# Kernel tuning notes

Hardware: AMD Instinct MI355X
Metric: run time of the kernel (lower is better)

The kernel has to match this reference:

```python
import jax, jax.numpy as jnp
import numpy as np

T, I, O = 10000, 2048, 512
DT = 0.001
PSP_DECAY = float(np.exp(-DT / 0.02))
OUT_DECAY = float(np.exp(-DT / 0.01))
STDP_C = 1.0
STDP_MU = 0.1
SPIKE_PROB = 0.05


def setup_inputs() -> dict:
    key = jax.random.key(0)
    k1, k2, k3 = jax.random.split(key, 3)
    # Poisson-encoded binary spike trains (as produced by SpikePopulationGroupBatchToTimeEncoder)
    input_spikes = (jax.random.uniform(k1, (T, I)) < SPIKE_PROB).astype(jnp.float32)
    u_rand = jax.random.uniform(k2, (T,), dtype=jnp.float32)  # per-step WTA sampling uniforms
    W = 0.1 * jax.random.normal(k3, (O, I), dtype=jnp.float32)
    b = jnp.zeros((O,), jnp.float32)
    return {"input_spikes": input_spikes, "u_rand": u_rand, "W": W, "b": b}


def _input_psp(spikes):
    # exponential PSP filter along time: psp[t] = decay*psp[t-1] + spikes[t]
    def step(c, s):
        c = PSP_DECAY * c + s
        return c, c
    _, psps = jax.lax.scan(step, jnp.zeros(spikes.shape[1], spikes.dtype), spikes)
    return psps  # [T, I]


def reference(input_spikes, u_rand, W, b):
    psps = _input_psp(input_spikes)
    n_out = W.shape[0]

    def step(carry, inp):
        W, b, trace = carry
        psp, u = inp
        z_in = W @ psp + b                              # linear, [O]
        p = jax.nn.softmax(z_in)                        # stochastic WTA cell
        idx = jnp.minimum(jnp.sum(jnp.cumsum(p) < u), n_out - 1)
        z_out = jax.nn.one_hot(idx, n_out, dtype=psp.dtype)
        trace = OUT_DECAY * trace + z_out               # neuron cell state
        # Bayesian STDP (sequential, depends on previous step's weights)
        dW = z_out[:, None] * (STDP_C * jnp.exp(-W) * psp[None, :] - 1.0)
        db = z_out * (STDP_C * jnp.exp(-b) - 1.0)
        return (W + STDP_MU * dW, b + STDP_MU * db, trace), z_out

    (Wf, bf, trace), z_outs = jax.lax.scan(
        step, (W, b, jnp.zeros_like(b)), (psps, u_rand))
    # matches torch forward's (stacked z_out, final z_state)
    return z_outs, trace
```

## Files before the change

### kernel.cpp

```cpp
#include <hip/hip_runtime.h>
#include <math.h>

static constexpr int T_STEPS = 10000;
static constexpr int I_DIM = 2048;
static constexpr int O_DIM = 512;
static constexpr int NWG = 4;
static constexpr int STRIPE = 128;
static constexpr int WGS = 512;
static constexpr int KPAD = 192;
static constexpr int GN = 16;
static constexpr float PSPD = 0.9512294245007140091f;
static constexpr float OUTD = 0.9048374180359595732f;
static constexpr float MU = 0.1f;

typedef float __attribute__((ext_vector_type(4))) f32x4;
typedef float __attribute__((ext_vector_type(2))) f32x2;

static constexpr size_t WT_BLK = (size_t)(I_DIM + 1) * STRIPE;

__global__ void build_idx_kernel(const float* __restrict__ spikes,
                                 unsigned short* __restrict__ idxl,
                                 int* __restrict__ cnts) {
    int t = blockIdx.x;
    int tid = threadIdx.x;
    if (t >= T_STEPS) {
        for (int p = tid; p < KPAD; p += 256) idxl[(size_t)t * KPAD + p] = (unsigned short)I_DIM;
        if (tid == 0) cnts[t] = 0;
        return;
    }
    const float4* row = reinterpret_cast<const float4*>(spikes + (size_t)t * I_DIM);
    float4 a = row[tid * 2];
    float4 b = row[tid * 2 + 1];
    float v[8] = {a.x, a.y, a.z, a.w, b.x, b.y, b.z, b.w};
    unsigned short tmp[8];
    int c = 0;
#pragma unroll
    for (int j = 0; j < 8; ++j)
        if (v[j] != 0.0f) tmp[c++] = (unsigned short)(tid * 8 + j);

    int lane = tid & 63, wid = tid >> 6;
    int x = c;
    for (int d = 1; d < 64; d <<= 1) {
        int y = __shfl_up(x, d);
        if (lane >= d) x += y;
    }
    __shared__ int wtot[4];
    if (lane == 63) wtot[wid] = x;
    __syncthreads();
    int off = x - c;
    for (int w = 0; w < wid; ++w) off += wtot[w];
    int tot = wtot[0] + wtot[1] + wtot[2] + wtot[3];
    if (tot > KPAD) tot = KPAD;
    for (int j = 0; j < c; ++j) {
        int p = off + j;
        if (p < KPAD) idxl[(size_t)t * KPAD + p] = tmp[j];
    }
    for (int p = tid; p < KPAD; p += 256)
        if (p >= tot) idxl[(size_t)t * KPAD + p] = (unsigned short)I_DIM;
    if (tid == 0) cnts[t] = tot;
}

__global__ void copy_w_kernel(const float* __restrict__ W, float* __restrict__ Wrow) {
    int i = blockIdx.x * blockDim.x + threadIdx.x;
    reinterpret_cast<float4*>(Wrow)[i] = reinterpret_cast<const float4*>(W)[i];
}

__global__ void transpose_kernel(const float* __restrict__ W, float* __restrict__ Wt) {
    __shared__ float tile[32][33];
    int i0 = blockIdx.x * 32;
    int o0 = blockIdx.y * 32;
    int x = threadIdx.x;
    for (int y = threadIdx.y; y < 32; y += 8)
        tile[y][x] = W[(size_t)(o0 + y) * I_DIM + i0 + x];
    __syncthreads();
    for (int y = threadIdx.y; y < 32; y += 8) {
        int o = o0 + x, i = i0 + y;
        Wt[(size_t)(o >> 7) * WT_BLK + (size_t)i * STRIPE + (o & 127)] = tile[x][y];
    }
}

__global__ void zero_pad_row_kernel(float* __restrict__ Wt) {
    int w = threadIdx.x >> 7, c = threadIdx.x & 127;
    Wt[(size_t)w * WT_BLK + (size_t)I_DIM * STRIPE + c] = 0.0f;
}

__device__ __forceinline__ void bar() {
    asm volatile("s_waitcnt lgkmcnt(0)" ::: "memory");
    __builtin_amdgcn_sched_barrier(0);
    __builtin_amdgcn_s_barrier();
    __builtin_amdgcn_sched_barrier(0);
}

__device__ __forceinline__ float wave_max_dpp(float x) {
    int xb = __float_as_int(x);
#define DPPSTEPM(ctrl, rm)                                                          \
    {                                                                               \
        int tt = __builtin_amdgcn_update_dpp(0xff800000, xb, ctrl, rm, 0xf, false); \
        xb = __float_as_int(fmaxf(__int_as_float(xb), __int_as_float(tt)));         \
    }
    DPPSTEPM(0x111, 0xf)
    DPPSTEPM(0x112, 0xf)
    DPPSTEPM(0x114, 0xf)
    DPPSTEPM(0x118, 0xf)
    DPPSTEPM(0x142, 0xa)
    DPPSTEPM(0x143, 0xc)
#undef DPPSTEPM
    return __int_as_float(__builtin_amdgcn_readlane(xb, 63));
}

__device__ __forceinline__ float dpp_scan_add(float x) {
#define DPPSTEPA(ctrl, rm)                                                          \
    {                                                                               \
        float tt = __int_as_float(                                                  \
            __builtin_amdgcn_update_dpp(0, __float_as_int(x), ctrl, rm, 0xf, false)); \
        x += tt;                                                                    \
    }
    DPPSTEPA(0x111, 0xf)
    DPPSTEPA(0x112, 0xf)
    DPPSTEPA(0x114, 0xf)
    DPPSTEPA(0x118, 0xf)
    DPPSTEPA(0x142, 0xa)
    DPPSTEPA(0x143, 0xc)
#undef DPPSTEPA
    return x;
}

__launch_bounds__(WGS, 1)
__global__ void seq_kernel(const unsigned short* __restrict__ idxl,
                           const int* __restrict__ cnts,
                           const float* __restrict__ u_rand,
                           const float* __restrict__ b_in,
                           float* __restrict__ Wrow,
                           float* __restrict__ Wt,
                           unsigned long long* __restrict__ slots,
                           float* __restrict__ out) {
    __shared__ __align__(16) float psp[I_DIM + 4];
    __shared__ __align__(16) float mk0[I_DIM + 4];
    __shared__ __align__(16) float mk1[I_DIM + 4];
    __shared__ f32x2 sg[8][64];
    __shared__ float redE[8], redF[8], redG[2][8];
    __shared__ unsigned short sidx[3][KPAD];
    __shared__ int s_rr, s_own;

    const int w = blockIdx.x;
    const int tid = threadIdx.x;
    const int lane = tid & 63;
    const int jw = tid >> 6;
    const int i4 = tid * 4;
    const int o0 = w * STRIPE;
    float* __restrict__ WtS = Wt + (size_t)w * WT_BLK;
    const unsigned long long wt_base = (unsigned long long)WtS;

    for (int p = tid; p < I_DIM + 4; p += WGS) { psp[p] = 0.0f; mk0[p] = 0.0f; mk1[p] = 0.0f; }
    for (int p = tid; p < 3 * KPAD; p += WGS) ((unsigned short*)sidx)[p] = idxl[p];
    if (tid == 0) { s_rr = 0; s_own = 0; }
    __syncthreads();
    const int cnt0 = cnts[0];
    if (tid < KPAD) {
        psp[sidx[0][tid]] = 1.0f;
        mk1[sidx[1][tid]] = 1.0f;
    }
    __syncthreads();
    {
        float a0 = 0.0f, a1 = 0.0f;
        for (int k = jw; k < cnt0; k += 8) {
            int col = sidx[0][k];
            f32x2 v = *(const f32x2*)(WtS + (size_t)col * STRIPE + lane * 2);
            a0 += v.x; a1 += v.y;
        }
        sg[jw][lane] = (f32x2){a0, a1};
    }
    float aA0 = 0.0f, aA1 = 0.0f, b0 = 0.0f, b1 = 0.0f, tr0 = 0.0f, tr1 = 0.0f;
    if (jw == 0) { b0 = b_in[o0 + 2 * lane]; b1 = b_in[o0 + 2 * lane + 1]; }
    int own1 = 0, own2 = 0, col1 = 0, col2 = 0;
    float nw0 = 0.0f, nw1 = 0.0f, nw2 = 0.0f, nw3 = 0.0f;
    int cnt_use = cnts[1];
    float u_cur = u_rand[0];
    __syncthreads();

    for (int t = 0; t < T_STEPS; ++t) {
        const int par = t & 1;
        float* mcur = par ? mk1 : mk0;
        float* mnxt = par ? mk0 : mk1;

        float u_nxt; int cnt_fut;
        {
            const float* up = u_rand + (t + 1 < T_STEPS ? t + 1 : T_STEPS - 1);
            asm volatile("global_load_dword %0, %1, off" : "=&v"(u_nxt) : "v"(up) : "memory");
            const int* cp = cnts + (t + 2);
            asm volatile("global_load_dword %0, %1, off" : "=&v"(cnt_fut) : "v"(cp) : "memory");
        }
        unsigned int pfw = 0;
        if (tid >= 256 && tid < 256 + KPAD / 2) {
            const unsigned int* pp = reinterpret_cast<const unsigned int*>(idxl) +
                                     (size_t)(t + 3) * (KPAD / 2) + (tid - 256);
            asm volatile("global_load_dword %0, %1, off" : "=&v"(pfw) : "v"(pp) : "memory");
        }
        f32x2 vals[GN];
        {
            const unsigned short* lst = sidx[(t + 1) % 3];
#pragma unroll
            for (int j = 0; j < GN; ++j) {
                int col = lst[jw + 8 * j];
                unsigned int voff = ((unsigned)col << 9) | ((unsigned)lane << 3);
                asm volatile("global_load_dwordx2 %0, %1, %2"
                             : "=&v"(vals[j]) : "v"(voff), "s"(wt_base) : "memory");
            }
        }
        f32x4 mreg = *(const f32x4*)(mnxt + i4);
        if (own1) {
            float gp2 = nw0 * mreg.x + nw1 * mreg.y + nw2 * mreg.z + nw3 * mreg.w;
            float gs = dpp_scan_add(gp2);
            if (lane == 63) redG[par][jw] = gs;
        }
        *(f32x4*)(mcur + i4) = (f32x4){0.0f, 0.0f, 0.0f, 0.0f};

        float e0 = 0.0f, e1 = 0.0f, pin = 0.0f, pex = 0.0f, m_w = 0.0f, S_w = 0.0f;
        if (jw == 0) {
            tr0 *= OUTD; tr1 *= OUTD;
            float v0 = 0.0f, v1 = 0.0f;
#pragma unroll
            for (int j = 0; j < 8; ++j) { f32x2 s = sg[j][lane]; v0 += s.x; v1 += s.y; }
            if (own1) {
                float es = 0.0f, fs = 0.0f;
#pragma unroll
                for (int j = 0; j < 8; ++j) { es += redE[j]; fs += redF[j]; }
                if (lane == (col1 >> 1)) {
                    if (col1 & 1) { aA1 += es; v1 = fs; } else { aA0 += es; v0 = fs; }
                }
            }
            if (own2 && !(own1 && col2 == col1)) {
                float gs = 0.0f;
#pragma unroll
                for (int j = 0; j < 8; ++j) gs += redG[par ^ 1][j];
                if (lane == (col2 >> 1)) { if (col2 & 1) v1 = gs; else v0 = gs; }
            }
            aA0 = PSPD * aA0 + v0; aA1 = PSPD * aA1 + v1;
            float z0 = aA0 + b0, z1 = aA1 + b1;
            m_w = wave_max_dpp(fmaxf(z0, z1));
            e0 = expf(z0 - m_w); e1 = expf(z1 - m_w);
            pin = dpp_scan_add(e0 + e1);
            pex = __int_as_float(
                __builtin_amdgcn_update_dpp(0, __float_as_int(pin), 0x111, 0xf, 0xf, false));
            float p15 = __int_as_float(__builtin_amdgcn_readlane(__float_as_int(pin), 15));
            float p31 = __int_as_float(__builtin_amdgcn_readlane(__float_as_int(pin), 31));
            float p47 = __int_as_float(__builtin_amdgcn_readlane(__float_as_int(pin), 47));
            if (lane == 16) pex = p15;
            if (lane == 32) pex = p31;
            if (lane == 48) pex = p47;
            S_w = __int_as_float(__builtin_amdgcn_readlane(__float_as_int(pin), 63));
            unsigned long long tag = ((unsigned long long)(unsigned)(t + 1)) << 32;
            if (lane == 0) {
                unsigned long long* my = slots + (((size_t)par * NWG + w) * 2);
                __hip_atomic_store(my + 0, tag | (unsigned)__float_as_int(m_w),
                                   __ATOMIC_RELAXED, __HIP_MEMORY_SCOPE_AGENT);
                __hip_atomic_store(my + 1, tag | (unsigned)__float_as_int(S_w),
                                   __ATOMIC_RELAXED, __HIP_MEMORY_SCOPE_AGENT);
            }
            int oi = lane >> 1; oi += (oi >= w) ? 1 : 0; oi &= 3;
            unsigned long long* sp = slots + (((size_t)par * NWG + oi) * 2 + (lane & 1));
            bool need = (lane < 6);
            unsigned long long want = (unsigned long long)(unsigned)(t + 1);
            unsigned long long got = 0;
            bool ok = !need;
            int it = 0;
            while (!__all(ok)) {
                if (!ok) {
                    got = __hip_atomic_load(sp, __ATOMIC_RELAXED, __HIP_MEMORY_SCOPE_AGENT);
                    ok = ((got >> 32) == want);
                }
                if (++it > (1 << 21)) break;
            }
            float pay = __int_as_float((int)(unsigned)got);
            float mj[4], sj[4];
#pragma unroll
            for (int j = 0; j < 4; ++j) {
                if (j == w) { mj[j] = m_w; sj[j] = S_w; }
                else {
                    int pos = j - (j > w ? 1 : 0);
                    mj[j] = __shfl(pay, 2 * pos);
                    sj[j] = __shfl(pay, 2 * pos + 1);
                }
            }
            float M = fmaxf(fmaxf(mj[0], mj[1]), fmaxf(mj[2], mj[3]));
            float o_run = 0.0f, offw = 0.0f, offn = 0.0f, sc_w = 0.0f;
#pragma unroll
            for (int j = 0; j < 4; ++j) {
                float sc = expf(mj[j] - M);
                if (j == w) { offw = o_run; sc_w = sc; }
                o_run = fmaf(sj[j], sc, o_run);
                if (j == w) offn = o_run;
            }
            float uQ = u_cur * o_run;
            int owner = (((offw < uQ) || w == 0) && ((uQ <= offn) || w == NWG - 1)) ? 1 : 0;
            if (lane == 0) { s_own = owner; s_rr = STRIPE - 1; }
            if (owner) {
                float cqp0 = fmaf(pex, sc_w, offw);
                float cq0  = fmaf(pex + e0, sc_w, offw);
                float cq1  = fmaf(pin, sc_w, offw);
                bool firstG = (w == 0 && lane == 0);
                bool lastG  = (w == NWG - 1 && lane == 63);
                bool w0c = (cqp0 < uQ || firstG) && (uQ <= cq0);
                bool w1c = (cq0 < uQ) && (uQ <= cq1 || lastG);
                if (w0c) s_rr = 2 * lane;
                if (w1c) s_rr = 2 * lane + 1;
            }
        }
        bar();

        const int rr = s_rr;
        const int own = s_own;
        const int rrglob = o0 + rr;
        f32x4 w2 = (f32x4){0.0f, 0.0f, 0.0f, 0.0f};
        if (own) {
            const float* rp = Wrow + (size_t)rrglob * I_DIM + i4;
            asm volatile("global_load_dwordx4 %0, %1, off" : "=&v"(w2) : "v"(rp) : "memory");
        }
        asm volatile("s_waitcnt vmcnt(0)" ::: "memory");
        __builtin_amdgcn_sched_barrier(0);
        asm volatile("" : "+v"(cnt_fut), "+v"(u_nxt));
        {
            float a0 = vals[0].x, a1 = vals[0].y;
#pragma unroll
            for (int j = 1; j < GN; ++j) { a0 += vals[j].x; a1 += vals[j].y; }
            if (cnt_use > 8 * GN) {
                const unsigned short* lst = sidx[(t + 1) % 3];
                for (int k = 8 * GN + jw; k < cnt_use; k += 8) {
                    int col = lst[k];
                    f32x2 v = *(const f32x2*)(WtS + (size_t)col * STRIPE + lane * 2);
                    a0 += v.x; a1 += v.y;
                }
            }
            sg[jw][lane] = (f32x2){a0, a1};
        }
        if (tid >= 256 && tid < 256 + KPAD / 2)
            ((unsigned int*)sidx[(t + 3) % 3])[tid - 256] = pfw;
        if (tid < KPAD) mcur[sidx[(t + 2) % 3][tid]] = 1.0f;
        f32x4 pr = *(const f32x4*)(psp + i4);
        if (own) {
            nw0 = w2.x + MU * (expf(-w2.x) * pr.x - 1.0f);
            nw1 = w2.y + MU * (expf(-w2.y) * pr.y - 1.0f);
            nw2 = w2.z + MU * (expf(-w2.z) * pr.z - 1.0f);
            nw3 = w2.w + MU * (expf(-w2.w) * pr.w - 1.0f);
            *(f32x4*)(Wrow + (size_t)rrglob * I_DIM + i4) = (f32x4){nw0, nw1, nw2, nw3};
            WtS[(size_t)(i4 + 0) * STRIPE + rr] = nw0;
            WtS[(size_t)(i4 + 1) * STRIPE + rr] = nw1;
            WtS[(size_t)(i4 + 2) * STRIPE + rr] = nw2;
            WtS[(size_t)(i4 + 3) * STRIPE + rr] = nw3;
            float dp = (nw0 - w2.x) * pr.x + (nw1 - w2.y) * pr.y +
                       (nw2 - w2.z) * pr.z + (nw3 - w2.w) * pr.w;
            float gp = nw0 * mreg.x + nw1 * mreg.y + nw2 * mreg.z + nw3 * mreg.w;
            float ds = dpp_scan_add(dp);
            float gs = dpp_scan_add(gp);
            if (lane == 63) { redE[jw] = ds; redF[jw] = gs; }
            if (jw == 0 && lane == (rr >> 1)) {
                if (rr & 1) { tr1 += 1.0f; b1 = b1 + MU * (expf(-b1) - 1.0f); }
                else        { tr0 += 1.0f; b0 = b0 + MU * (expf(-b0) - 1.0f); }
                out[(size_t)t * O_DIM + rrglob] = 1.0f;
            }
        }
        {
#pragma clang fp contract(off)
            float q0 = pr.x * PSPD; q0 += mreg.x;
            float q1 = pr.y * PSPD; q1 += mreg.y;
            float q2 = pr.z * PSPD; q2 += mreg.z;
            float q3 = pr.w * PSPD; q3 += mreg.w;
            *(f32x4*)(psp + i4) = (f32x4){q0, q1, q2, q3};
        }
        own2 = own1; col2 = col1;
        own1 = own;  col1 = rr;
        cnt_use = cnt_fut;
        u_cur = u_nxt;
        bar();
    }

    if (jw == 0) {
        out[(size_t)T_STEPS * O_DIM + o0 + 2 * lane] = tr0;
        out[(size_t)T_STEPS * O_DIM + o0 + 2 * lane + 1] = tr1;
    }
}

extern "C" void kernel_launch(void* const* d_in, const int* in_sizes, int n_in,
                              void* d_out, int out_size, void* d_ws, size_t ws_size,
                              hipStream_t stream) {
    const float* spikes = (const float*)d_in[0];
    const float* u_rand = (const float*)d_in[1];
    const float* W      = (const float*)d_in[2];
    const float* b      = (const float*)d_in[3];
    float* out = (float*)d_out;

    float* Wrow = (float*)d_ws;
    float* Wt   = Wrow + (size_t)O_DIM * I_DIM;
    unsigned short* idxl = (unsigned short*)(Wt + (size_t)NWG * WT_BLK);
    int* cnts = (int*)(idxl + (size_t)(T_STEPS + 4) * KPAD);
    unsigned long long* slots = (unsigned long long*)(cnts + (T_STEPS + 4));

    hipMemsetAsync(d_out, 0, (size_t)out_size * sizeof(float), stream);
    hipMemsetAsync(slots, 0, 2 * NWG * 2 * sizeof(unsigned long long), stream);

    hipLaunchKernelGGL(build_idx_kernel, dim3(T_STEPS + 4), dim3(256), 0, stream,
                       spikes, idxl, cnts);
    hipLaunchKernelGGL(copy_w_kernel, dim3((O_DIM * I_DIM / 4) / 256), dim3(256), 0, stream,
                       W, Wrow);
    hipLaunchKernelGGL(transpose_kernel, dim3(I_DIM / 32, O_DIM / 32), dim3(32, 8), 0, stream,
                       W, Wt);
    hipLaunchKernelGGL(zero_pad_row_kernel, dim3(1), dim3(NWG * STRIPE), 0, stream, Wt);
    hipLaunchKernelGGL(seq_kernel, dim3(NWG), dim3(WGS), 0, stream,
                       idxl, cnts, u_rand, b, Wrow, Wt, slots, out);
}
```

Baseline: 34.54 ms.

## Dedicate wave 0 to softmax/WTA while seven waves gather next-step partial sums

The per-step work is split by wave. Wave 0 only does the softmax, the cross-workgroup exchange and the WTA sampling. The other seven waves gather the next step's sparse weight-column sums into a double-buffered shared array, and they also do the PSP and mask updates before the barrier. This moves the gather and the PSP update off the critical path after the barrier, so they overlap with wave 0's serial reduction and spin-wait. In exchange, the gather is spread over fewer waves, each doing more loads per step (GN raised to 19), and the spin-wait iteration limit is doubled.

```diff
diff --git a/kernel.cpp b/kernel.cpp
--- a/kernel.cpp
+++ b/kernel.cpp
@@ -8,7 +8,8 @@
 static constexpr int STRIPE = 128;
 static constexpr int WGS = 512;
 static constexpr int KPAD = 192;
-static constexpr int GN = 16;
+static constexpr int NSPL = 7;
+static constexpr int GN = 19;
 static constexpr float PSPD = 0.9512294245007140091f;
 static constexpr float OUTD = 0.9048374180359595732f;
 static constexpr float MU = 0.1f;
@@ -137,7 +138,7 @@
     __shared__ __align__(16) float psp[I_DIM + 4];
     __shared__ __align__(16) float mk0[I_DIM + 4];
     __shared__ __align__(16) float mk1[I_DIM + 4];
-    __shared__ f32x2 sg[8][64];
+    __shared__ f32x2 sg[2][NSPL][64];
     __shared__ float redE[8], redF[8], redG[2][8];
     __shared__ unsigned short sidx[3][KPAD];
     __shared__ int s_rr, s_own;
@@ -161,14 +162,14 @@
         mk1[sidx[1][tid]] = 1.0f;
     }
     __syncthreads();
-    {
+    if (jw > 0) {
         float a0 = 0.0f, a1 = 0.0f;
-        for (int k = jw; k < cnt0; k += 8) {
+        for (int k = jw - 1; k < cnt0; k += NSPL) {
             int col = sidx[0][k];
             f32x2 v = *(const f32x2*)(WtS + (size_t)col * STRIPE + lane * 2);
             a0 += v.x; a1 += v.y;
         }
-        sg[jw][lane] = (f32x2){a0, a1};
+        sg[0][jw - 1][lane] = (f32x2){a0, a1};
     }
     float aA0 = 0.0f, aA1 = 0.0f, b0 = 0.0f, b1 = 0.0f, tr0 = 0.0f, tr1 = 0.0f;
     if (jw == 0) { b0 = b_in[o0 + 2 * lane]; b1 = b_in[o0 + 2 * lane + 1]; }
@@ -180,6 +181,8 @@
 
     for (int t = 0; t < T_STEPS; ++t) {
         const int par = t & 1;
+        const int cb = par;
+        const int nb = par ^ 1;
         float* mcur = par ? mk1 : mk0;
         float* mnxt = par ? mk0 : mk1;
 
@@ -196,31 +199,62 @@
                                      (size_t)(t + 3) * (KPAD / 2) + (tid - 256);
             asm volatile("global_load_dword %0, %1, off" : "=&v"(pfw) : "v"(pp) : "memory");
         }
-        f32x2 vals[GN];
-        {
-            const unsigned short* lst = sidx[(t + 1) % 3];
-#pragma unroll
-            for (int j = 0; j < GN; ++j) {
-                int col = lst[jw + 8 * j];
-                unsigned int voff = ((unsigned)col << 9) | ((unsigned)lane << 3);
-                asm volatile("global_load_dwordx2 %0, %1, %2"
-                             : "=&v"(vals[j]) : "v"(voff), "s"(wt_base) : "memory");
-            }
-        }
-        f32x4 mreg = *(const f32x4*)(mnxt + i4);
-        if (own1) {
-            float gp2 = nw0 * mreg.x + nw1 * mreg.y + nw2 * mreg.z + nw3 * mreg.w;
-            float gs = dpp_scan_add(gp2);
-            if (lane == 63) redG[par][jw] = gs;
-        }
-        *(f32x4*)(mcur + i4) = (f32x4){0.0f, 0.0f, 0.0f, 0.0f};
-
-        float e0 = 0.0f, e1 = 0.0f, pin = 0.0f, pex = 0.0f, m_w = 0.0f, S_w = 0.0f;
-        if (jw == 0) {
+        f32x4 mreg = (f32x4){0.0f, 0.0f, 0.0f, 0.0f};
+        f32x4 pr = (f32x4){0.0f, 0.0f, 0.0f, 0.0f};
+
+        if (jw > 0) {
+            f32x2 vals[GN];
+            {
+                const unsigned short* lst = sidx[(t + 1) % 3];
+                const int kw = jw - 1;
+#pragma unroll
+                for (int j = 0; j < GN; ++j) {
+                    int col = lst[kw + NSPL * j];
+                    unsigned int voff = ((unsigned)col << 9) | ((unsigned)lane << 3);
+                    asm volatile("global_load_dwordx2 %0, %1, %2"
+                                 : "=&v"(vals[j]) : "v"(voff), "s"(wt_base) : "memory");
+                }
+            }
+            mreg = *(const f32x4*)(mnxt + i4);
+            if (own1) {
+                float gp2 = nw0 * mreg.x + nw1 * mreg.y + nw2 * mreg.z + nw3 * mreg.w;
+                float gs = dpp_scan_add(gp2);
+                if (lane == 63) redG[par][jw] = gs;
+            }
+            *(f32x4*)(mcur + i4) = (f32x4){0.0f, 0.0f, 0.0f, 0.0f};
+            pr = *(const f32x4*)(psp + i4);
+            {
+#pragma clang fp contract(off)
+                float q0 = pr.x * PSPD; q0 += mreg.x;
+                float q1 = pr.y * PSPD; q1 += mreg.y;
+                float q2 = pr.z * PSPD; q2 += mreg.z;
+                float q3 = pr.w * PSPD; q3 += mreg.w;
+                *(f32x4*)(psp + i4) = (f32x4){q0, q1, q2, q3};
+            }
+            asm volatile("s_waitcnt vmcnt(0)" ::: "memory");
+            __builtin_amdgcn_sched_barrier(0);
+            asm volatile("" : "+v"(cnt_fut), "+v"(u_nxt));
+            {
+                float a0 = vals[0].x, a1 = vals[0].y;
+#pragma unroll
+                for (int j = 1; j < GN; ++j) { a0 += vals[j].x; a1 += vals[j].y; }
+                if (cnt_use > NSPL * GN) {
+                    const unsigned short* lst = sidx[(t + 1) % 3];
+                    for (int k = NSPL * GN + (jw - 1); k < cnt_use; k += NSPL) {
+                        int col = lst[k];
+                        f32x2 v = *(const f32x2*)(WtS + (size_t)col * STRIPE + lane * 2);
+                        a0 += v.x; a1 += v.y;
+                    }
+                }
+                sg[nb][jw - 1][lane] = (f32x2){a0, a1};
+            }
+            if (tid >= 256 && tid < 256 + KPAD / 2)
+                ((unsigned int*)sidx[(t + 3) % 3])[tid - 256] = pfw;
+        } else {
             tr0 *= OUTD; tr1 *= OUTD;
             float v0 = 0.0f, v1 = 0.0f;
 #pragma unroll
-            for (int j = 0; j < 8; ++j) { f32x2 s = sg[j][lane]; v0 += s.x; v1 += s.y; }
+            for (int j = 0; j < NSPL; ++j) { f32x2 s = sg[cb][j][lane]; v0 += s.x; v1 += s.y; }
             if (own1) {
                 float es = 0.0f, fs = 0.0f;
 #pragma unroll
@@ -237,10 +271,10 @@
             }
             aA0 = PSPD * aA0 + v0; aA1 = PSPD * aA1 + v1;
             float z0 = aA0 + b0, z1 = aA1 + b1;
-            m_w = wave_max_dpp(fmaxf(z0, z1));
-            e0 = expf(z0 - m_w); e1 = expf(z1 - m_w);
-            pin = dpp_scan_add(e0 + e1);
-            pex = __int_as_float(
+            float m_w = wave_max_dpp(fmaxf(z0, z1));
+            float e0 = expf(z0 - m_w), e1 = expf(z1 - m_w);
+            float pin = dpp_scan_add(e0 + e1);
+            float pex = __int_as_float(
                 __builtin_amdgcn_update_dpp(0, __float_as_int(pin), 0x111, 0xf, 0xf, false));
             float p15 = __int_as_float(__builtin_amdgcn_readlane(__float_as_int(pin), 15));
             float p31 = __int_as_float(__builtin_amdgcn_readlane(__float_as_int(pin), 31));
@@ -248,7 +282,7 @@
             if (lane == 16) pex = p15;
             if (lane == 32) pex = p31;
             if (lane == 48) pex = p47;
-            S_w = __int_as_float(__builtin_amdgcn_readlane(__float_as_int(pin), 63));
+            float S_w = __int_as_float(__builtin_amdgcn_readlane(__float_as_int(pin), 63));
             unsigned long long tag = ((unsigned long long)(unsigned)(t + 1)) << 32;
             if (lane == 0) {
                 unsigned long long* my = slots + (((size_t)par * NWG + w) * 2);
@@ -269,7 +303,7 @@
                     got = __hip_atomic_load(sp, __ATOMIC_RELAXED, __HIP_MEMORY_SCOPE_AGENT);
                     ok = ((got >> 32) == want);
                 }
-                if (++it > (1 << 21)) break;
+                if (++it > (1 << 22)) break;
             }
             float pay = __int_as_float((int)(unsigned)got);
             float mj[4], sj[4];
@@ -305,6 +339,25 @@
                 if (w0c) s_rr = 2 * lane;
                 if (w1c) s_rr = 2 * lane + 1;
             }
+            asm volatile("s_waitcnt vmcnt(0)" ::: "memory");
+            __builtin_amdgcn_sched_barrier(0);
+            asm volatile("" : "+v"(cnt_fut), "+v"(u_nxt));
+            mreg = *(const f32x4*)(mnxt + i4);
+            if (own1) {
+                float gp2 = nw0 * mreg.x + nw1 * mreg.y + nw2 * mreg.z + nw3 * mreg.w;
+                float gs = dpp_scan_add(gp2);
+                if (lane == 63) redG[par][0] = gs;
+            }
+            *(f32x4*)(mcur + i4) = (f32x4){0.0f, 0.0f, 0.0f, 0.0f};
+            pr = *(const f32x4*)(psp + i4);
+            {
+#pragma clang fp contract(off)
+                float q0 = pr.x * PSPD; q0 += mreg.x;
+                float q1 = pr.y * PSPD; q1 += mreg.y;
+                float q2 = pr.z * PSPD; q2 += mreg.z;
+                float q3 = pr.w * PSPD; q3 += mreg.w;
+                *(f32x4*)(psp + i4) = (f32x4){q0, q1, q2, q3};
+            }
         }
         bar();
 
@@ -316,28 +369,10 @@
             const float* rp = Wrow + (size_t)rrglob * I_DIM + i4;
             asm volatile("global_load_dwordx4 %0, %1, off" : "=&v"(w2) : "v"(rp) : "memory");
         }
-        asm volatile("s_waitcnt vmcnt(0)" ::: "memory");
-        __builtin_amdgcn_sched_barrier(0);
-        asm volatile("" : "+v"(cnt_fut), "+v"(u_nxt));
-        {
-            float a0 = vals[0].x, a1 = vals[0].y;
-#pragma unroll
-            for (int j = 1; j < GN; ++j) { a0 += vals[j].x; a1 += vals[j].y; }
-            if (cnt_use > 8 * GN) {
-                const unsigned short* lst = sidx[(t + 1) % 3];
-                for (int k = 8 * GN + jw; k < cnt_use; k += 8) {
-                    int col = lst[k];
-                    f32x2 v = *(const f32x2*)(WtS + (size_t)col * STRIPE + lane * 2);
-                    a0 += v.x; a1 += v.y;
-                }
-            }
-            sg[jw][lane] = (f32x2){a0, a1};
-        }
-        if (tid >= 256 && tid < 256 + KPAD / 2)
-            ((unsigned int*)sidx[(t + 3) % 3])[tid - 256] = pfw;
         if (tid < KPAD) mcur[sidx[(t + 2) % 3][tid]] = 1.0f;
-        f32x4 pr = *(const f32x4*)(psp + i4);
         if (own) {
+            asm volatile("s_waitcnt vmcnt(0)" ::: "memory");
+            __builtin_amdgcn_sched_barrier(0);
             nw0 = w2.x + MU * (expf(-w2.x) * pr.x - 1.0f);
             nw1 = w2.y + MU * (expf(-w2.y) * pr.y - 1.0f);
             nw2 = w2.z + MU * (expf(-w2.z) * pr.z - 1.0f);
@@ -359,14 +394,6 @@
                 out[(size_t)t * O_DIM + rrglob] = 1.0f;
             }
         }
-        {
-#pragma clang fp contract(off)
-            float q0 = pr.x * PSPD; q0 += mreg.x;
-            float q1 = pr.y * PSPD; q1 += mreg.y;
-            float q2 = pr.z * PSPD; q2 += mreg.z;
-            float q3 = pr.w * PSPD; q3 += mreg.w;
-            *(f32x4*)(psp + i4) = (f32x4){q0, q1, q2, q3};
-        }
         own2 = own1; col2 = col1;
         own1 = own;  col1 = rr;
         cnt_use = cnt_fut;
```

Result: faster. 27.75 ms (-19.6%).

## Collapse four-workgroup split into single 1024-thread workgroup, dropping global-memory handshakes

Applied to the files above, without the earlier changes.

Replaces the four cooperating workgroups, which exchanged per-step softmax max/sum through global atomic slots with spin-waits, with one 1024-thread workgroup that does the whole output dimension and reduces through shared memory and barriers. Work inside the block is specialised: 12 waves gather transposed weight rows with dwordx4 loads over six splits, and 4 waves do softmax and sampling, with winner selection via shared atomicMin. This removes cross-CU polling latency on every sequential step. In exchange, one CU now carries all gather bandwidth and weight-update work, so per-step compute and memory issue are less parallel.

```diff
diff --git a/kernel.cpp b/kernel.cpp
--- a/kernel.cpp
+++ b/kernel.cpp
@@ -4,19 +4,16 @@
 static constexpr int T_STEPS = 10000;
 static constexpr int I_DIM = 2048;
 static constexpr int O_DIM = 512;
-static constexpr int NWG = 4;
-static constexpr int STRIPE = 128;
-static constexpr int WGS = 512;
+static constexpr int WGS = 1024;
 static constexpr int KPAD = 192;
-static constexpr int GN = 16;
+static constexpr int NSPL = 6;
+static constexpr int GN = 19;
 static constexpr float PSPD = 0.9512294245007140091f;
 static constexpr float OUTD = 0.9048374180359595732f;
 static constexpr float MU = 0.1f;
 
 typedef float __attribute__((ext_vector_type(4))) f32x4;
 typedef float __attribute__((ext_vector_type(2))) f32x2;
-
-static constexpr size_t WT_BLK = (size_t)(I_DIM + 1) * STRIPE;
 
 __global__ void build_idx_kernel(const float* __restrict__ spikes,
                                  unsigned short* __restrict__ idxl,
@@ -73,15 +70,12 @@
     for (int y = threadIdx.y; y < 32; y += 8)
         tile[y][x] = W[(size_t)(o0 + y) * I_DIM + i0 + x];
     __syncthreads();
-    for (int y = threadIdx.y; y < 32; y += 8) {
-        int o = o0 + x, i = i0 + y;
-        Wt[(size_t)(o >> 7) * WT_BLK + (size_t)i * STRIPE + (o & 127)] = tile[x][y];
-    }
+    for (int y = threadIdx.y; y < 32; y += 8)
+        Wt[(size_t)(i0 + y) * O_DIM + o0 + x] = tile[x][y];
 }
 
 __global__ void zero_pad_row_kernel(float* __restrict__ Wt) {
-    int w = threadIdx.x >> 7, c = threadIdx.x & 127;
-    Wt[(size_t)w * WT_BLK + (size_t)I_DIM * STRIPE + c] = 0.0f;
+    Wt[(size_t)I_DIM * O_DIM + threadIdx.x] = 0.0f;
 }
 
 __device__ __forceinline__ void bar() {
@@ -132,28 +126,32 @@
                            const float* __restrict__ b_in,
                            float* __restrict__ Wrow,
                            float* __restrict__ Wt,
-                           unsigned long long* __restrict__ slots,
                            float* __restrict__ out) {
     __shared__ __align__(16) float psp[I_DIM + 4];
     __shared__ __align__(16) float mk0[I_DIM + 4];
     __shared__ __align__(16) float mk1[I_DIM + 4];
-    __shared__ f32x2 sg[8][64];
-    __shared__ float redE[8], redF[8], redG[2][8];
-    __shared__ unsigned short sidx[3][KPAD];
-    __shared__ int s_rr, s_own;
-
-    const int w = blockIdx.x;
+    __shared__ f32x4 sg[2][NSPL][128];
+    __shared__ float redE[16], redF[16], redG[2][16];
+    __shared__ float redM[4], redS[4];
+    __shared__ __align__(16) unsigned short sidx[3][KPAD];
+    __shared__ int s_rr;
+
     const int tid = threadIdx.x;
     const int lane = tid & 63;
     const int jw = tid >> 6;
-    const int i4 = tid * 4;
-    const int o0 = w * STRIPE;
-    float* __restrict__ WtS = Wt + (size_t)w * WT_BLK;
-    const unsigned long long wt_base = (unsigned long long)WtS;
+    const int i2 = tid * 2;
+    const int gt = tid - 256;
+    const int r = gt >> 7;
+    const int g = gt & 127;
+    const f32x4* __restrict__ Wt4 = reinterpret_cast<const f32x4*>(Wt);
+    const unsigned long long wt_base = (unsigned long long)Wt;
 
     for (int p = tid; p < I_DIM + 4; p += WGS) { psp[p] = 0.0f; mk0[p] = 0.0f; mk1[p] = 0.0f; }
-    for (int p = tid; p < 3 * KPAD; p += WGS) ((unsigned short*)sidx)[p] = idxl[p];
-    if (tid == 0) { s_rr = 0; s_own = 0; }
+    if (tid < 3 * KPAD) ((unsigned short*)sidx)[tid] = idxl[tid];
+    if (tid < 16) { redE[tid] = 0.0f; redF[tid] = 0.0f; }
+    if (tid < 32) redG[tid >> 4][tid & 15] = 0.0f;
+    if (tid < 4) { redM[tid] = 0.0f; redS[tid] = 0.0f; }
+    if (tid == 0) s_rr = O_DIM - 1;
     __syncthreads();
     const int cnt0 = cnts[0];
     if (tid < KPAD) {
@@ -161,83 +159,113 @@
         mk1[sidx[1][tid]] = 1.0f;
     }
     __syncthreads();
-    {
-        float a0 = 0.0f, a1 = 0.0f;
-        for (int k = jw; k < cnt0; k += 8) {
-            int col = sidx[0][k];
-            f32x2 v = *(const f32x2*)(WtS + (size_t)col * STRIPE + lane * 2);
-            a0 += v.x; a1 += v.y;
-        }
-        sg[jw][lane] = (f32x2){a0, a1};
+    if (tid >= 256) {
+        f32x4 acc = {0.0f, 0.0f, 0.0f, 0.0f};
+        for (int k = r; k < cnt0; k += NSPL)
+            acc += Wt4[(size_t)sidx[0][k] * 128 + g];
+        sg[0][r][g] = acc;
     }
     float aA0 = 0.0f, aA1 = 0.0f, b0 = 0.0f, b1 = 0.0f, tr0 = 0.0f, tr1 = 0.0f;
-    if (jw == 0) { b0 = b_in[o0 + 2 * lane]; b1 = b_in[o0 + 2 * lane + 1]; }
-    int own1 = 0, own2 = 0, col1 = 0, col2 = 0;
-    float nw0 = 0.0f, nw1 = 0.0f, nw2 = 0.0f, nw3 = 0.0f;
-    int cnt_use = cnts[1];
-    float u_cur = u_rand[0];
+    if (jw < 4) { b0 = b_in[jw * 128 + 2 * lane]; b1 = b_in[jw * 128 + 2 * lane + 1]; }
+    int col1 = 1 << 30, col2 = 1 << 30;
+    float nw0 = 0.0f, nw1 = 0.0f;
+    int cnt_use = cnts[1], cnt_fut = 0;
+    float u_cur = u_rand[0], u_nxt = 0.0f;
+    unsigned int pfw = 0;
     __syncthreads();
 
     for (int t = 0; t < T_STEPS; ++t) {
-        const int par = t & 1;
+        const int par = t & 1, cb = par, nb = par ^ 1;
         float* mcur = par ? mk1 : mk0;
         float* mnxt = par ? mk0 : mk1;
 
-        float u_nxt; int cnt_fut;
+        f32x2 mreg = *(const f32x2*)(mnxt + i2);
         {
-            const float* up = u_rand + (t + 1 < T_STEPS ? t + 1 : T_STEPS - 1);
-            asm volatile("global_load_dword %0, %1, off" : "=&v"(u_nxt) : "v"(up) : "memory");
-            const int* cp = cnts + (t + 2);
-            asm volatile("global_load_dword %0, %1, off" : "=&v"(cnt_fut) : "v"(cp) : "memory");
-        }
-        unsigned int pfw = 0;
-        if (tid >= 256 && tid < 256 + KPAD / 2) {
-            const unsigned int* pp = reinterpret_cast<const unsigned int*>(idxl) +
-                                     (size_t)(t + 3) * (KPAD / 2) + (tid - 256);
-            asm volatile("global_load_dword %0, %1, off" : "=&v"(pfw) : "v"(pp) : "memory");
-        }
-        f32x2 vals[GN];
+            float gp2 = nw0 * mreg.x + nw1 * mreg.y;
+            float s2 = dpp_scan_add(gp2);
+            if (lane == 63) redG[par][jw] = s2;
+        }
+        mcur[i2] = 0.0f; mcur[i2 + 1] = 0.0f;
+        f32x2 pr = *(const f32x2*)(psp + i2);
         {
-            const unsigned short* lst = sidx[(t + 1) % 3];
-#pragma unroll
-            for (int j = 0; j < GN; ++j) {
-                int col = lst[jw + 8 * j];
-                unsigned int voff = ((unsigned)col << 9) | ((unsigned)lane << 3);
-                asm volatile("global_load_dwordx2 %0, %1, %2"
-                             : "=&v"(vals[j]) : "v"(voff), "s"(wt_base) : "memory");
-            }
-        }
-        f32x4 mreg = *(const f32x4*)(mnxt + i4);
-        if (own1) {
-            float gp2 = nw0 * mreg.x + nw1 * mreg.y + nw2 * mreg.z + nw3 * mreg.w;
-            float gs = dpp_scan_add(gp2);
-            if (lane == 63) redG[par][jw] = gs;
-        }
-        *(f32x4*)(mcur + i4) = (f32x4){0.0f, 0.0f, 0.0f, 0.0f};
-
-        float e0 = 0.0f, e1 = 0.0f, pin = 0.0f, pex = 0.0f, m_w = 0.0f, S_w = 0.0f;
-        if (jw == 0) {
+#pragma clang fp contract(off)
+            float q0 = pr.x * PSPD; q0 += mreg.x;
+            float q1 = pr.y * PSPD; q1 += mreg.y;
+            psp[i2] = q0; psp[i2 + 1] = q1;
+        }
+        if (tid == 0) s_rr = O_DIM - 1;
+
+        float e0 = 0.0f, e1 = 0.0f, pin = 0.0f, pex = 0.0f;
+        if (tid >= 256) {
+            {
+                const int* cp = cnts + (t + 2);
+                asm volatile("global_load_dword %0, %1, off" : "=&v"(cnt_fut) : "v"(cp) : "memory");
+            }
+            if (gt < KPAD / 2) {
+                const unsigned int* pp = reinterpret_cast<const unsigned int*>(idxl) +
+                                         (size_t)(t + 3) * (KPAD / 2) + gt;
+                asm volatile("global_load_dword %0, %1, off" : "=&v"(pfw) : "v"(pp) : "memory");
+            }
+            f32x4 vals[GN];
+            {
+                const unsigned short* lst = sidx[(t + 1) % 3];
+#pragma unroll
+                for (int j = 0; j < GN; ++j) {
+                    int col = lst[r + NSPL * j];
+                    unsigned int voff = ((unsigned)col << 11) + ((unsigned)g << 4);
+                    asm volatile("global_load_dwordx4 %0, %1, %2"
+                                 : "=&v"(vals[j]) : "v"(voff), "s"(wt_base) : "memory");
+                }
+            }
+            asm volatile("s_waitcnt vmcnt(0)" ::: "memory");
+            __builtin_amdgcn_sched_barrier(0);
+            asm volatile("" : "+v"(cnt_fut), "+v"(pfw));
+            {
+                f32x4 acc = vals[0];
+#pragma unroll
+                for (int j = 1; j < GN; ++j) acc += vals[j];
+                if (cnt_use > NSPL * GN) {
+                    const unsigned short* lst = sidx[(t + 1) % 3];
+                    for (int k = NSPL * GN + r; k < cnt_use; k += NSPL)
+                        acc += Wt4[(size_t)lst[k] * 128 + g];
+                }
+                sg[nb][r][g] = acc;
+            }
+            if (gt < KPAD / 2)
+                ((unsigned int*)sidx[(t + 3) % 3])[gt] = pfw;
+        } else {
+            {
+                int tu = t + 1; if (tu > T_STEPS - 1) tu = T_STEPS - 1;
+                const float* up = u_rand + tu;
+                asm volatile("global_load_dword %0, %1, off" : "=&v"(u_nxt) : "v"(up) : "memory");
+            }
             tr0 *= OUTD; tr1 *= OUTD;
             float v0 = 0.0f, v1 = 0.0f;
 #pragma unroll
-            for (int j = 0; j < 8; ++j) { f32x2 s = sg[j][lane]; v0 += s.x; v1 += s.y; }
-            if (own1) {
+            for (int r2 = 0; r2 < NSPL; ++r2) {
+                const f32x2* sgc = reinterpret_cast<const f32x2*>(&sg[cb][r2][0]);
+                f32x2 s2v = sgc[jw * 64 + lane];
+                v0 += s2v.x; v1 += s2v.y;
+            }
+            if ((col1 >> 7) == jw) {
                 float es = 0.0f, fs = 0.0f;
 #pragma unroll
-                for (int j = 0; j < 8; ++j) { es += redE[j]; fs += redF[j]; }
-                if (lane == (col1 >> 1)) {
-                    if (col1 & 1) { aA1 += es; v1 = fs; } else { aA0 += es; v0 = fs; }
+                for (int j = 0; j < 16; ++j) { es += redE[j]; fs += redF[j]; }
+                int c1 = col1 & 127;
+                if (lane == (c1 >> 1)) {
+                    if (c1 & 1) { aA1 += es; v1 = fs; } else { aA0 += es; v0 = fs; }
                 }
             }
-            if (own2 && !(own1 && col2 == col1)) {
+            if (((col2 >> 7) == jw) && col2 != col1) {
                 float gs = 0.0f;
 #pragma unroll
-                for (int j = 0; j < 8; ++j) gs += redG[par ^ 1][j];
-                if (lane == (col2 >> 1)) { if (col2 & 1) v1 = gs; else v0 = gs; }
+                for (int j = 0; j < 16; ++j) gs += redG[par ^ 1][j];
+                int c2 = col2 & 127;
+                if (lane == (c2 >> 1)) { if (c2 & 1) v1 = gs; else v0 = gs; }
             }
             aA0 = PSPD * aA0 + v0; aA1 = PSPD * aA1 + v1;
             float z0 = aA0 + b0, z1 = aA1 + b1;
-            m_w = wave_max_dpp(fmaxf(z0, z1));
+            float m_w = wave_max_dpp(fmaxf(z0, z1));
             e0 = expf(z0 - m_w); e1 = expf(z1 - m_w);
             pin = dpp_scan_add(e0 + e1);
             pex = __int_as_float(
@@ -248,135 +276,75 @@
             if (lane == 16) pex = p15;
             if (lane == 32) pex = p31;
             if (lane == 48) pex = p47;
-            S_w = __int_as_float(__builtin_amdgcn_readlane(__float_as_int(pin), 63));
-            unsigned long long tag = ((unsigned long long)(unsigned)(t + 1)) << 32;
-            if (lane == 0) {
-                unsigned long long* my = slots + (((size_t)par * NWG + w) * 2);
-                __hip_atomic_store(my + 0, tag | (unsigned)__float_as_int(m_w),
-                                   __ATOMIC_RELAXED, __HIP_MEMORY_SCOPE_AGENT);
-                __hip_atomic_store(my + 1, tag | (unsigned)__float_as_int(S_w),
-                                   __ATOMIC_RELAXED, __HIP_MEMORY_SCOPE_AGENT);
-            }
-            int oi = lane >> 1; oi += (oi >= w) ? 1 : 0; oi &= 3;
-            unsigned long long* sp = slots + (((size_t)par * NWG + oi) * 2 + (lane & 1));
-            bool need = (lane < 6);
-            unsigned long long want = (unsigned long long)(unsigned)(t + 1);
-            unsigned long long got = 0;
-            bool ok = !need;
-            int it = 0;
-            while (!__all(ok)) {
-                if (!ok) {
-                    got = __hip_atomic_load(sp, __ATOMIC_RELAXED, __HIP_MEMORY_SCOPE_AGENT);
-                    ok = ((got >> 32) == want);
-                }
-                if (++it > (1 << 21)) break;
-            }
-            float pay = __int_as_float((int)(unsigned)got);
+            float S_w = __int_as_float(__builtin_amdgcn_readlane(__float_as_int(pin), 63));
+            if (lane == 0) { redM[jw] = m_w; redS[jw] = S_w; }
+        }
+        bar();
+
+        if (jw < 4) {
             float mj[4], sj[4];
 #pragma unroll
-            for (int j = 0; j < 4; ++j) {
-                if (j == w) { mj[j] = m_w; sj[j] = S_w; }
-                else {
-                    int pos = j - (j > w ? 1 : 0);
-                    mj[j] = __shfl(pay, 2 * pos);
-                    sj[j] = __shfl(pay, 2 * pos + 1);
-                }
-            }
+            for (int j = 0; j < 4; ++j) { mj[j] = redM[j]; sj[j] = redS[j]; }
             float M = fmaxf(fmaxf(mj[0], mj[1]), fmaxf(mj[2], mj[3]));
-            float o_run = 0.0f, offw = 0.0f, offn = 0.0f, sc_w = 0.0f;
+            float o_run = 0.0f, offw = 0.0f, sc_w = 0.0f;
 #pragma unroll
             for (int j = 0; j < 4; ++j) {
                 float sc = expf(mj[j] - M);
-                if (j == w) { offw = o_run; sc_w = sc; }
+                if (j == jw) { offw = o_run; sc_w = sc; }
                 o_run = fmaf(sj[j], sc, o_run);
-                if (j == w) offn = o_run;
             }
             float uQ = u_cur * o_run;
-            int owner = (((offw < uQ) || w == 0) && ((uQ <= offn) || w == NWG - 1)) ? 1 : 0;
-            if (lane == 0) { s_own = owner; s_rr = STRIPE - 1; }
-            if (owner) {
-                float cqp0 = fmaf(pex, sc_w, offw);
-                float cq0  = fmaf(pex + e0, sc_w, offw);
-                float cq1  = fmaf(pin, sc_w, offw);
-                bool firstG = (w == 0 && lane == 0);
-                bool lastG  = (w == NWG - 1 && lane == 63);
-                bool w0c = (cqp0 < uQ || firstG) && (uQ <= cq0);
-                bool w1c = (cq0 < uQ) && (uQ <= cq1 || lastG);
-                if (w0c) s_rr = 2 * lane;
-                if (w1c) s_rr = 2 * lane + 1;
-            }
+            float cqp0 = fmaf(pex, sc_w, offw);
+            float cq0  = fmaf(pex + e0, sc_w, offw);
+            float cq1  = fmaf(pin, sc_w, offw);
+            bool firstG = (jw == 0 && lane == 0);
+            bool lastG  = (jw == 3 && lane == 63);
+            bool w0c = (cqp0 < uQ || firstG) && (uQ <= cq0);
+            bool w1c = (cq0 < uQ) && (uQ <= cq1 || lastG);
+            if (w0c) atomicMin(&s_rr, jw * 128 + 2 * lane);
+            if (w1c) atomicMin(&s_rr, jw * 128 + 2 * lane + 1);
+            asm volatile("s_waitcnt vmcnt(0)" ::: "memory");
+            __builtin_amdgcn_sched_barrier(0);
+            asm volatile("" : "+v"(u_nxt));
+            u_cur = u_nxt;
         }
         bar();
 
         const int rr = s_rr;
-        const int own = s_own;
-        const int rrglob = o0 + rr;
-        f32x4 w2 = (f32x4){0.0f, 0.0f, 0.0f, 0.0f};
-        if (own) {
-            const float* rp = Wrow + (size_t)rrglob * I_DIM + i4;
-            asm volatile("global_load_dwordx4 %0, %1, off" : "=&v"(w2) : "v"(rp) : "memory");
-        }
+        f32x2 w2v;
+        {
+            const float* rp0 = Wrow + (size_t)rr * I_DIM + i2;
+            asm volatile("global_load_dwordx2 %0, %1, off" : "=&v"(w2v) : "v"(rp0) : "memory");
+        }
+        if (tid < KPAD) mcur[sidx[(t + 2) % 3][tid]] = 1.0f;
         asm volatile("s_waitcnt vmcnt(0)" ::: "memory");
         __builtin_amdgcn_sched_barrier(0);
-        asm volatile("" : "+v"(cnt_fut), "+v"(u_nxt));
+        nw0 = w2v.x + MU * (expf(-w2v.x) * pr.x - 1.0f);
+        nw1 = w2v.y + MU * (expf(-w2v.y) * pr.y - 1.0f);
+        *reinterpret_cast<float2*>(&Wrow[(size_t)rr * I_DIM + i2]) = make_float2(nw0, nw1);
+        Wt[(size_t)i2 * O_DIM + rr] = nw0;
+        Wt[(size_t)(i2 + 1) * O_DIM + rr] = nw1;
         {
-            float a0 = vals[0].x, a1 = vals[0].y;
-#pragma unroll
-            for (int j = 1; j < GN; ++j) { a0 += vals[j].x; a1 += vals[j].y; }
-            if (cnt_use > 8 * GN) {
-                const unsigned short* lst = sidx[(t + 1) % 3];
-                for (int k = 8 * GN + jw; k < cnt_use; k += 8) {
-                    int col = lst[k];
-                    f32x2 v = *(const f32x2*)(WtS + (size_t)col * STRIPE + lane * 2);
-                    a0 += v.x; a1 += v.y;
-                }
-            }
-            sg[jw][lane] = (f32x2){a0, a1};
-        }
-        if (tid >= 256 && tid < 256 + KPAD / 2)
-            ((unsigned int*)sidx[(t + 3) % 3])[tid - 256] = pfw;
-        if (tid < KPAD) mcur[sidx[(t + 2) % 3][tid]] = 1.0f;
-        f32x4 pr = *(const f32x4*)(psp + i4);
-        if (own) {
-            nw0 = w2.x + MU * (expf(-w2.x) * pr.x - 1.0f);
-            nw1 = w2.y + MU * (expf(-w2.y) * pr.y - 1.0f);
-            nw2 = w2.z + MU * (expf(-w2.z) * pr.z - 1.0f);
-            nw3 = w2.w + MU * (expf(-w2.w) * pr.w - 1.0f);
-            *(f32x4*)(Wrow + (size_t)rrglob * I_DIM + i4) = (f32x4){nw0, nw1, nw2, nw3};
-            WtS[(size_t)(i4 + 0) * STRIPE + rr] = nw0;
-            WtS[(size_t)(i4 + 1) * STRIPE + rr] = nw1;
-            WtS[(size_t)(i4 + 2) * STRIPE + rr] = nw2;
-            WtS[(size_t)(i4 + 3) * STRIPE + rr] = nw3;
-            float dp = (nw0 - w2.x) * pr.x + (nw1 - w2.y) * pr.y +
-                       (nw2 - w2.z) * pr.z + (nw3 - w2.w) * pr.w;
-            float gp = nw0 * mreg.x + nw1 * mreg.y + nw2 * mreg.z + nw3 * mreg.w;
-            float ds = dpp_scan_add(dp);
-            float gs = dpp_scan_add(gp);
-            if (lane == 63) { redE[jw] = ds; redF[jw] = gs; }
-            if (jw == 0 && lane == (rr >> 1)) {
-                if (rr & 1) { tr1 += 1.0f; b1 = b1 + MU * (expf(-b1) - 1.0f); }
-                else        { tr0 += 1.0f; b0 = b0 + MU * (expf(-b0) - 1.0f); }
-                out[(size_t)t * O_DIM + rrglob] = 1.0f;
-            }
-        }
-        {
-#pragma clang fp contract(off)
-            float q0 = pr.x * PSPD; q0 += mreg.x;
-            float q1 = pr.y * PSPD; q1 += mreg.y;
-            float q2 = pr.z * PSPD; q2 += mreg.z;
-            float q3 = pr.w * PSPD; q3 += mreg.w;
-            *(f32x4*)(psp + i4) = (f32x4){q0, q1, q2, q3};
-        }
-        own2 = own1; col2 = col1;
-        own1 = own;  col1 = rr;
+            float dp = (nw0 - w2v.x) * pr.x + (nw1 - w2v.y) * pr.y;
+            float gp = nw0 * mreg.x + nw1 * mreg.y;
+            float sd = dpp_scan_add(dp);
+            float sf = dpp_scan_add(gp);
+            if (lane == 63) { redE[jw] = sd; redF[jw] = sf; }
+        }
+        if (jw == (rr >> 7) && lane == ((rr & 127) >> 1)) {
+            if (rr & 1) { tr1 += 1.0f; b1 = b1 + MU * (expf(-b1) - 1.0f); }
+            else        { tr0 += 1.0f; b0 = b0 + MU * (expf(-b0) - 1.0f); }
+            out[(size_t)t * O_DIM + rr] = 1.0f;
+        }
+        col2 = col1; col1 = rr;
         cnt_use = cnt_fut;
-        u_cur = u_nxt;
         bar();
     }
 
-    if (jw == 0) {
-        out[(size_t)T_STEPS * O_DIM + o0 + 2 * lane] = tr0;
-        out[(size_t)T_STEPS * O_DIM + o0 + 2 * lane + 1] = tr1;
+    __syncthreads();
+    if (jw < 4) {
+        out[(size_t)T_STEPS * O_DIM + jw * 128 + 2 * lane] = tr0;
+        out[(size_t)T_STEPS * O_DIM + jw * 128 + 2 * lane + 1] = tr1;
     }
 }
 
@@ -391,12 +359,10 @@
 
     float* Wrow = (float*)d_ws;
     float* Wt   = Wrow + (size_t)O_DIM * I_DIM;
-    unsigned short* idxl = (unsigned short*)(Wt + (size_t)NWG * WT_BLK);
+    unsigned short* idxl = (unsigned short*)(Wt + (size_t)(I_DIM + 1) * O_DIM);
     int* cnts = (int*)(idxl + (size_t)(T_STEPS + 4) * KPAD);
-    unsigned long long* slots = (unsigned long long*)(cnts + (T_STEPS + 4));
 
     hipMemsetAsync(d_out, 0, (size_t)out_size * sizeof(float), stream);
-    hipMemsetAsync(slots, 0, 2 * NWG * 2 * sizeof(unsigned long long), stream);
 
     hipLaunchKernelGGL(build_idx_kernel, dim3(T_STEPS + 4), dim3(256), 0, stream,
                        spikes, idxl, cnts);
@@ -404,7 +370,7 @@
                        W, Wrow);
     hipLaunchKernelGGL(transpose_kernel, dim3(I_DIM / 32, O_DIM / 32), dim3(32, 8), 0, stream,
                        W, Wt);
-    hipLaunchKernelGGL(zero_pad_row_kernel, dim3(1), dim3(NWG * STRIPE), 0, stream, Wt);
-    hipLaunchKernelGGL(seq_kernel, dim3(NWG), dim3(WGS), 0, stream,
-                       idxl, cnts, u_rand, b, Wrow, Wt, slots, out);
-}
+    hipLaunchKernelGGL(zero_pad_row_kernel, dim3(1), dim3(O_DIM), 0, stream, Wt);
+    hipLaunchKernelGGL(seq_kernel, dim3(1), dim3(WGS), 0, stream,
+                       idxl, cnts, u_rand, b, Wrow, Wt, out);
+}
```

Measured after the change: 37.89 ms. 1.1x slower.
